# Performance work log

Measured on AMD Instinct MI355X. Metric: run time of the kernel, lower is better.

The kernel has to match this reference:

```python
import jax, jax.numpy as jnp
import numpy as np

C = 512
G = 32  # GroupNorm groups
EPS = 1e-6


def setup_inputs() -> dict:
    key = jax.random.key(0)
    ks = jax.random.split(key, 12)
    B, H, W = 2, 64, 64
    s = 0.02
    return {
        "x": jax.random.normal(ks[0], (B, C, H, W), dtype=jnp.float32),
        "gn_w": jnp.ones((C,), jnp.float32),
        "gn_b": jnp.zeros((C,), jnp.float32),
        "wq": jax.random.normal(ks[1], (C, C), jnp.float32) * s,
        "bq": jnp.zeros((C,), jnp.float32),
        "wk": jax.random.normal(ks[2], (C, C), jnp.float32) * s,
        "bk": jnp.zeros((C,), jnp.float32),
        "wv": jax.random.normal(ks[3], (C, C), jnp.float32) * s,
        "bv": jnp.zeros((C,), jnp.float32),
        "wp": jax.random.normal(ks[4], (C, C), jnp.float32) * s,
        "bp": jnp.zeros((C,), jnp.float32),
    }


def _group_norm(x, w, b):
    B, Cc, H, W = x.shape
    xg = x.reshape(B, G, Cc // G, H, W)
    mu = jnp.mean(xg, axis=(2, 3, 4), keepdims=True)
    var = jnp.var(xg, axis=(2, 3, 4), keepdims=True)
    xn = ((xg - mu) * jax.lax.rsqrt(var + EPS)).reshape(B, Cc, H, W)
    return xn * w[None, :, None, None] + b[None, :, None, None]


def reference(x, gn_w, gn_b, wq, bq, wk, bk, wv, bv, wp, bp):
    B, Cc, H, W = x.shape
    N = H * W
    h = _group_norm(x, gn_w, gn_b)
    hf = h.reshape(B, Cc, N)  # [B,C,N]
    # 1x1 conv == per-position linear over channels
    q = jnp.einsum('dc,bcn->bdn', wq, hf) + bq[None, :, None]
    k = jnp.einsum('dc,bcn->bdn', wk, hf) + bk[None, :, None]
    v = jnp.einsum('dc,bcn->bdn', wv, hf) + bv[None, :, None]
    scale = float(Cc) ** -0.5
    # scores[b,q_pos,k_pos]
    w_ = jnp.einsum('bcq,bck->bqk', q, k) * scale
    w_ = jax.nn.softmax(w_, axis=2)
    # h_[b,c,q] = sum_k v[b,c,k] * w_[b,q,k]
    o = jnp.einsum('bck,bqk->bcq', v, w_)
    o = jnp.einsum('dc,bcn->bdn', wp, o) + bp[None, :, None]
    return x + o.reshape(B, Cc, H, W)
```

## Files before the change

### kernel.cpp

```cpp
#include <hip/hip_runtime.h>


typedef unsigned short u16;
typedef unsigned int u32;
typedef unsigned char u8;
typedef float f32x4 __attribute__((ext_vector_type(4)));
typedef long l2 __attribute__((ext_vector_type(2)));

#define NPOS 4096
#define CCH 512

__device__ __forceinline__ int kperm(int k) {
  return (k & ~0x78) | ((k >> 2) & 0x18) | ((k << 2) & 0x60);
}

__device__ __forceinline__ u16 f2bf(float f) {
  u32 u = __builtin_bit_cast(u32, f);
  u += 0x7fffu + ((u >> 16) & 1u);
  return (u16)(u >> 16);
}
__device__ __forceinline__ float bf2f(u16 h) {
  u32 u = ((u32)h) << 16;
  return __builtin_bit_cast(float, u);
}
__device__ __forceinline__ u8 f2fp8(float f) {
  u32 pk = __builtin_amdgcn_cvt_pk_fp8_f32(f, f, 0, false);
  return (u8)(pk & 0xff);
}

__device__ __forceinline__ void load16_lds8(const u8* g, u8* l) {
  __builtin_amdgcn_global_load_lds(
      (const __attribute__((address_space(1))) void*)g,
      (__attribute__((address_space(3))) void*)l, 16, 0, 0);
}

__global__ __launch_bounds__(256) void gn_stats_part(const float* __restrict__ x,
                                                     float2* __restrict__ part) {
  int id = blockIdx.x;
  const float4* p = (const float4*)(x + (size_t)id * 16384);
  float s = 0.f, s2 = 0.f;
  for (int i = threadIdx.x; i < 4096; i += 256) {
    float4 u = p[i];
    s += u.x + u.y + u.z + u.w;
    s2 += u.x * u.x + u.y * u.y + u.z * u.z + u.w * u.w;
  }
  for (int o = 32; o; o >>= 1) {
    s += __shfl_xor(s, o);
    s2 += __shfl_xor(s2, o);
  }
  __shared__ float rs[4], rq[4];
  int lane = threadIdx.x & 63, w = threadIdx.x >> 6;
  if (lane == 0) { rs[w] = s; rq[w] = s2; }
  __syncthreads();
  if (threadIdx.x == 0)
    part[id] = make_float2(rs[0] + rs[1] + rs[2] + rs[3], rq[0] + rq[1] + rq[2] + rq[3]);
}

__global__ __launch_bounds__(256) void gn_apply8(const float* __restrict__ x,
                                                 const float* __restrict__ gnw,
                                                 const float* __restrict__ gnb,
                                                 const float2* __restrict__ pstats,
                                                 u8* __restrict__ h8) {
  int b = blockIdx.z, c0 = blockIdx.y * 64, n0 = blockIdx.x * 64;
  __shared__ u8 lt[64][80];
  const float* xb = x + (size_t)b * CCH * NPOS;
  int tid = threadIdx.x;
#pragma unroll
  for (int it = 0; it < 4; ++it) {
    int ci = (tid >> 4) + it * 16;
    int nj = (tid & 15) * 4;
    int c = c0 + ci;
    float4 v = *(const float4*)&xb[(size_t)c * NPOS + n0 + nj];
    const float2* pp = pstats + ((size_t)b * 32 + (c >> 4)) * 4;
    float s = pp[0].x + pp[1].x + pp[2].x + pp[3].x;
    float s2 = pp[0].y + pp[1].y + pp[2].y + pp[3].y;
    float mu = s * (1.f / 65536.f);
    float var = s2 * (1.f / 65536.f) - mu * mu;
    float rst = rsqrtf(var + 1e-6f);
    float w = gnw[c] * rst;
    float bb = gnb[c] - mu * w;
    lt[nj + 0][ci] = f2fp8(v.x * w + bb);
    lt[nj + 1][ci] = f2fp8(v.y * w + bb);
    lt[nj + 2][ci] = f2fp8(v.z * w + bb);
    lt[nj + 3][ci] = f2fp8(v.w * w + bb);
  }
  __syncthreads();
  int ni = tid >> 2, c16 = (tid & 3) * 16;
  uint4 o = *(const uint4*)&lt[ni][c16];
  u8* row = h8 + ((size_t)b * NPOS + n0 + ni) * CCH;
  int pc = kperm(c0 + c16);
  *(uint2*)&row[pc] = make_uint2(o.x, o.y);
  *(uint2*)&row[kperm(c0 + c16 + 8)] = make_uint2(o.z, o.w);
}

__global__ __launch_bounds__(256) void wconv8(const float* __restrict__ w0,
                                              const float* __restrict__ w1,
                                              const float* __restrict__ w2,
                                              const float* __restrict__ w3,
                                              u8* __restrict__ dst,
                                              const float* __restrict__ bq,
                                              const float* __restrict__ bk,
                                              const float* __restrict__ bv,
                                              float* __restrict__ bqkv) {
  int which = blockIdx.y;
  int bx = blockIdx.x;
  int t = threadIdx.x;
  if (bx == 256) {
    if (which < 3) {
      const float* bsrc = which == 0 ? bq : which == 1 ? bk : bv;
      bqkv[which * 512 + t] = bsrc[t];
      bqkv[which * 512 + 256 + t] = bsrc[256 + t];
    }
    return;
  }
  const float* src = which == 0 ? w0 : which == 1 ? w1 : which == 2 ? w2 : w3;
  u8* d = dst + (size_t)which * (CCH * CCH);
  int i = bx * 256 + t;
  float4 v = ((const float4*)src)[i];
  u32 pk = __builtin_amdgcn_cvt_pk_fp8_f32(v.x, v.y, 0, false);
  pk = __builtin_amdgcn_cvt_pk_fp8_f32(v.z, v.w, pk, true);
  int byte = i * 4;
  int c = byte & 511;
  ((u32*)d)[((byte & ~511) | kperm(c)) >> 2] = pk;
}

template <int EPI, bool SWIZ>
__global__ __launch_bounds__(256, 4) void gemm_f8(const u8* __restrict__ A,
                                                  const u8* __restrict__ Bm,
                                                  void* __restrict__ Cv,
                                                  const float* __restrict__ bias,
                                                  const float* __restrict__ resid,
                                                  float* __restrict__ lpart,
                                                  float alpha, int K,
                                                  int lda, int ldb, int ldc,
                                                  long sA, long sB, long sC, long sR) {
  const int b = blockIdx.z;
  int bx = blockIdx.x, by = blockIdx.y;
  if (SWIZ) {
    int id = by * gridDim.x + bx;
    int g = id >> 8;
    int w = id & 255;
    bx = (g << 3) | (w & 7);
    by = w >> 3;
  }
  A += (size_t)b * sA;
  Bm += (size_t)b * sB;
  const int m0 = by * 128, n0 = bx * 128;
  __shared__ u8 sAt[128 * 128];
  __shared__ u8 sBt[128 * 128];
  const int tid = threadIdx.x, wave = tid >> 6, lane = tid & 63;
  const int lrow = lane & 15, kch = lane >> 4;
  const int wm = (wave >> 1) * 64, wn = (wave & 1) * 64;
  const int srow = lane >> 3;
  const int sseg = ((lane & 7) ^ srow) * 16;
  f32x4 acc[4][4] = {};

  for (int k0 = 0; k0 < K; k0 += 128) {
#pragma unroll
    for (int r = 0; r < 4; ++r) {
      int ch = wave * 4 + r;
      load16_lds8(A + (size_t)(m0 + ch * 8 + srow) * lda + (k0 + sseg), sAt + ch * 1024);
      load16_lds8(Bm + (size_t)(n0 + ch * 8 + srow) * ldb + (k0 + sseg), sBt + ch * 1024);
    }
    __syncthreads();
#pragma unroll
    for (int kkhi = 0; kkhi < 2; ++kkhi) {
      const int slot = (kch << 1) | kkhi;
      l2 af[4], bf[4];
#pragma unroll
      for (int i = 0; i < 4; ++i) {
        int ra = wm + i * 16 + lrow;
        af[i] = *(const l2*)(sAt + ra * 128 + ((slot ^ (ra & 7)) << 4));
        int rb = wn + i * 16 + lrow;
        bf[i] = *(const l2*)(sBt + rb * 128 + ((slot ^ (rb & 7)) << 4));
      }
#pragma unroll
      for (int i = 0; i < 4; ++i)
#pragma unroll
        for (int j = 0; j < 4; ++j)
          acc[i][j] =
              __builtin_amdgcn_mfma_f32_16x16x32_fp8_fp8(af[i].x, bf[j].x, acc[i][j], 0, 0, 0);
#pragma unroll
      for (int i = 0; i < 4; ++i)
#pragma unroll
        for (int j = 0; j < 4; ++j)
          acc[i][j] =
              __builtin_amdgcn_mfma_f32_16x16x32_fp8_fp8(af[i].y, bf[j].y, acc[i][j], 0, 0, 0);
    }
    __syncthreads();
  }

  const int col = lane & 15, rbase = (lane >> 4) * 4;
  const size_t cb = (size_t)b * sC;
  float rsum[4][4];
  if (EPI == 2) {
#pragma unroll
    for (int i = 0; i < 4; ++i)
#pragma unroll
      for (int r = 0; r < 4; ++r) rsum[i][r] = 0.f;
  }
#pragma unroll
  for (int i = 0; i < 4; ++i) {
    int mrow = m0 + wm + i * 16 + rbase;
#pragma unroll
    for (int j = 0; j < 4; ++j) {
      int ncol = n0 + wn + j * 16 + col;
      float bcol = (EPI == 0) ? bias[ncol] : 0.f;
      int scol = ncol;
      if (EPI == 0 && ncol < 1024) scol = kperm(ncol);
      if (EPI == 2) scol = kperm(ncol);
#pragma unroll
      for (int r = 0; r < 4; ++r) {
        int m = mrow + r;
        float v = acc[i][j][r];
        if (EPI == 0) {
          ((u8*)Cv)[cb + (size_t)m * ldc + scol] = f2fp8(v + bcol);
        } else if (EPI == 1) {
          v = v * alpha + bias[m] + resid[(size_t)b * sR + (size_t)m * ldc + ncol];
          ((float*)Cv)[cb + (size_t)m * ldc + ncol] = v;
        } else {
          float s = fminf(fmaxf(v * alpha, -14.f), 6.49f);
          float e = exp2f(s);
          rsum[i][r] += e;
          ((u8*)Cv)[cb + (size_t)m * ldc + scol] = f2fp8(4.f * e);
        }
      }
    }
  }
  if (EPI == 2) {
#pragma unroll
    for (int i = 0; i < 4; ++i) {
#pragma unroll
      for (int r = 0; r < 4; ++r) {
        float v = rsum[i][r];
        v += __shfl_xor(v, 1);
        v += __shfl_xor(v, 2);
        v += __shfl_xor(v, 4);
        v += __shfl_xor(v, 8);
        if ((lane & 15) == 0) {
          int m = m0 + wm + i * 16 + rbase + r;
          lpart[((size_t)b * NPOS + m) * 64 + bx * 2 + (wave & 1)] = v;
        }
      }
    }
  }
}

__global__ __launch_bounds__(256, 4) void gemm_pv_fp8(const u8* __restrict__ Um,
                                                      const u8* __restrict__ Vm,
                                                      u16* __restrict__ part,
                                                      const float* __restrict__ lpart,
                                                      float* __restrict__ lsum) {
  const int b = blockIdx.z >> 2, slice = blockIdx.z & 3;
  const int id = blockIdx.x + (blockIdx.y << 2);
  const int xcd = id & 7, j = id >> 3;
  const int bx = j & 3, by = xcd + ((j >> 2) << 3);
  const u8* A = Um + (size_t)b * ((size_t)NPOS * NPOS) + (size_t)slice * 1024;
  const u8* Bv = Vm + (size_t)b * (CCH * NPOS) + (size_t)slice * 1024;
  const int m0 = by * 128, n0 = bx * 128;
  __shared__ u8 sA[128 * 128];
  __shared__ u8 sB[128 * 128];
  const int tid = threadIdx.x, wave = tid >> 6, lane = tid & 63;
  const int lrow = lane & 15, kch = lane >> 4;
  const int wm = (wave >> 1) * 64, wn = (wave & 1) * 64;
  const int srow = lane >> 3;
  const int sseg = ((lane & 7) ^ srow) * 16;
  f32x4 acc[4][4] = {};

  for (int k0 = 0; k0 < 1024; k0 += 128) {
#pragma unroll
    for (int r = 0; r < 4; ++r) {
      int ch = wave * 4 + r;
      load16_lds8(A + (size_t)(m0 + ch * 8 + srow) * NPOS + (k0 + sseg), sA + ch * 1024);
      load16_lds8(Bv + (size_t)(n0 + ch * 8 + srow) * NPOS + (k0 + sseg), sB + ch * 1024);
    }
    __syncthreads();
#pragma unroll
    for (int kkhi = 0; kkhi < 2; ++kkhi) {
      const int slot = (kch << 1) | kkhi;
      l2 af[4], bf[4];
#pragma unroll
      for (int i = 0; i < 4; ++i) {
        int ra = wm + i * 16 + lrow;
        af[i] = *(const l2*)(sA + ra * 128 + ((slot ^ (ra & 7)) << 4));
        int rb = wn + i * 16 + lrow;
        bf[i] = *(const l2*)(sB + rb * 128 + ((slot ^ (rb & 7)) << 4));
      }
#pragma unroll
      for (int i = 0; i < 4; ++i)
#pragma unroll
        for (int jj = 0; jj < 4; ++jj)
          acc[i][jj] =
              __builtin_amdgcn_mfma_f32_16x16x32_fp8_fp8(af[i].x, bf[jj].x, acc[i][jj], 0, 0, 0);
#pragma unroll
      for (int i = 0; i < 4; ++i)
#pragma unroll
        for (int jj = 0; jj < 4; ++jj)
          acc[i][jj] =
              __builtin_amdgcn_mfma_f32_16x16x32_fp8_fp8(af[i].y, bf[jj].y, acc[i][jj], 0, 0, 0);
    }
    __syncthreads();
  }

  const int col = lane & 15, rbase = (lane >> 4) * 4;
  u16* dst = part + (size_t)slice * ((size_t)2 * NPOS * CCH) + (size_t)b * (NPOS * CCH);
#pragma unroll
  for (int i = 0; i < 4; ++i) {
    int mrow = m0 + wm + i * 16 + rbase;
#pragma unroll
    for (int jj = 0; jj < 4; ++jj) {
      int ncol = n0 + wn + jj * 16 + col;
#pragma unroll
      for (int r = 0; r < 4; ++r)
        dst[(size_t)(mrow + r) * CCH + ncol] = f2bf(acc[i][jj][r]);
    }
  }
  if (bx == 0 && tid < 128) {
    const float* lp = lpart + ((size_t)b * NPOS + m0 + tid) * 64;
    float s = 0.f;
#pragma unroll
    for (int c = 0; c < 64; ++c) s += lp[c];
    lsum[(size_t)b * NPOS + m0 + tid] = s;
  }
}

__global__ __launch_bounds__(256) void merge_pv8(const u16* __restrict__ part,
                                                 const float* __restrict__ lsum,
                                                 u8* __restrict__ dst) {
  const long sl = 4194304;
  int i = blockIdx.x * 256 + threadIdx.x;
  long e0 = (long)i * 8;
  int q = (int)((e0 >> 9) & 4095);
  int b = (int)(e0 >> 21);
  int c8 = (int)(e0 & 511);
  float inv = 8.f / lsum[(size_t)b * NPOS + q];
  uint4 a = ((const uint4*)part)[i];
  uint4 bb = ((const uint4*)(part + sl))[i];
  uint4 c = ((const uint4*)(part + 2 * sl))[i];
  uint4 d = ((const uint4*)(part + 3 * sl))[i];
  u32 wa[4] = {a.x, a.y, a.z, a.w}, wb_[4] = {bb.x, bb.y, bb.z, bb.w};
  u32 wc[4] = {c.x, c.y, c.z, c.w}, wd[4] = {d.x, d.y, d.z, d.w};
  float v[8];
#pragma unroll
  for (int j = 0; j < 4; ++j) {
    v[2 * j] = (bf2f((u16)(wa[j] & 0xffff)) + bf2f((u16)(wb_[j] & 0xffff)) +
                bf2f((u16)(wc[j] & 0xffff)) + bf2f((u16)(wd[j] & 0xffff))) * inv;
    v[2 * j + 1] = (bf2f((u16)(wa[j] >> 16)) + bf2f((u16)(wb_[j] >> 16)) +
                    bf2f((u16)(wc[j] >> 16)) + bf2f((u16)(wd[j] >> 16))) * inv;
  }
  uint2 o;
  u32 p0 = __builtin_amdgcn_cvt_pk_fp8_f32(v[0], v[1], 0, false);
  p0 = __builtin_amdgcn_cvt_pk_fp8_f32(v[2], v[3], p0, true);
  u32 p1 = __builtin_amdgcn_cvt_pk_fp8_f32(v[4], v[5], 0, false);
  p1 = __builtin_amdgcn_cvt_pk_fp8_f32(v[6], v[7], p1, true);
  o.x = p0;
  o.y = p1;
  *(uint2*)&dst[((size_t)b * NPOS + q) * CCH + kperm(c8)] = o;
}

__global__ __launch_bounds__(256) void transpose_v8(const u8* __restrict__ src,
                                                    u8* __restrict__ dst, int srcld) {
  int b = blockIdx.z, n0 = blockIdx.x * 64, d0 = blockIdx.y * 64;
  __shared__ u8 lt[64][80];
  const u8* s = src + (size_t)b * NPOS * srcld;
  u8* d = dst + (size_t)b * CCH * NPOS;
  int t = threadIdx.x;
  {
    int r = t >> 2, c16 = (t & 3) * 16;
    uint4 v = *(const uint4*)&s[(size_t)(n0 + r) * srcld + d0 + c16];
    *(uint4*)&lt[r][c16] = v;
  }
  __syncthreads();
  {
    int dr = t >> 2, c16 = (t & 3) * 16;
    u8 tmp[16];
#pragma unroll
    for (int j = 0; j < 16; ++j) tmp[j] = lt[c16 + j][dr];
    uint4 o = *(uint4*)tmp;
    u8* row = d + (size_t)(d0 + dr) * NPOS;
    *(uint2*)&row[kperm(n0 + c16)] = make_uint2(o.x, o.y);
    *(uint2*)&row[kperm(n0 + c16 + 8)] = make_uint2(o.z, o.w);
  }
}

extern "C" void kernel_launch(void* const* d_in, const int* in_sizes, int n_in,
                              void* d_out, int out_size, void* d_ws, size_t ws_size,
                              hipStream_t stream) {
  const float* x = (const float*)d_in[0];
  const float* gnw = (const float*)d_in[1];
  const float* gnb = (const float*)d_in[2];
  const float* wq = (const float*)d_in[3];
  const float* bq = (const float*)d_in[4];
  const float* wk = (const float*)d_in[5];
  const float* bk = (const float*)d_in[6];
  const float* wv = (const float*)d_in[7];
  const float* bv = (const float*)d_in[8];
  const float* wp = (const float*)d_in[9];
  const float* bp = (const float*)d_in[10];
  float* out = (float*)d_out;

  char* ws = (char*)d_ws;
  size_t off = 0;
  auto alloc = [&](size_t bytes) {
    void* p = ws + off;
    off += (bytes + 1023) & ~(size_t)1023;
    return p;
  };
  float2* pstats = (float2*)alloc(256 * sizeof(float2));
  u8* w8 = (u8*)alloc((size_t)4 * CCH * CCH);
  u8* wp8 = w8 + 3 * CCH * CCH;
  float* bqkv = (float*)alloc(1536 * sizeof(float));
  u8* h8 = (u8*)alloc((size_t)2 * NPOS * CCH);
  u8* qkv8 = (u8*)alloc((size_t)2 * NPOS * 1536);
  u8* v8 = (u8*)alloc((size_t)2 * CCH * NPOS);
  u8* U8 = (u8*)alloc((size_t)2 * NPOS * NPOS);
  float* lpart = (float*)alloc((size_t)2 * NPOS * 64 * 4);
  float* lsum = (float*)alloc((size_t)2 * NPOS * 4);
  u16* part_pv = (u16*)alloc((size_t)4 * 2 * NPOS * CCH * 2);
  u8* o8 = (u8*)alloc((size_t)2 * NPOS * CCH);

  const long sHC8 = (long)NPOS * CCH;
  const long sQKV8 = (long)NPOS * 1536;
  const long sSS8 = (long)NPOS * NPOS;
  const long sOUT = (long)CCH * NPOS;
  const float scale2 = 0.044194173824159216f * 1.4426950408889634f;

  gn_stats_part<<<256, 256, 0, stream>>>(x, pstats);
  gn_apply8<<<dim3(64, 8, 2), 256, 0, stream>>>(x, gnw, gnb, pstats, h8);
  wconv8<<<dim3(257, 4), 256, 0, stream>>>(wq, wk, wv, wp, w8, bq, bk, bv, bqkv);
  gemm_f8<0, false><<<dim3(12, 32, 2), 256, 0, stream>>>(
      h8, w8, qkv8, bqkv, nullptr, nullptr, 1.f, CCH, CCH, CCH, 1536,
      sHC8, 0, sQKV8, 0);
  transpose_v8<<<dim3(64, 8, 2), 256, 0, stream>>>(qkv8 + 1024, v8, 1536);
  gemm_f8<2, true><<<dim3(32, 32, 2), 256, 0, stream>>>(
      qkv8, qkv8 + 512, U8, nullptr, nullptr, lpart, scale2, CCH, 1536, 1536, NPOS,
      sQKV8, sQKV8, sSS8, 0);
  gemm_pv_fp8<<<dim3(4, 32, 8), 256, 0, stream>>>(U8, v8, part_pv, lpart, lsum);
  merge_pv8<<<2048, 256, 0, stream>>>(part_pv, lsum, o8);
  gemm_f8<1, false><<<dim3(32, 4, 2), 256, 0, stream>>>(
      wp8, o8, out, bp, x, nullptr, 1.f / 32.f, CCH, CCH, CCH, NPOS,
      0, sHC8, sOUT, sOUT);
}
```

Measured before the change: 200.9 us.

## Use 32x32x64 scaled MFMA with pre-tiled fragment layouts for attention GEMMs

Replaces the 16x16x32 fp8 MFMA kernels for QK^T and PV with a new gemm_mx kernel that uses the MI355 scaled 32x32x64 f8f6f4 MFMA instruction. Q, K, V-transposed and the score matrix are written directly in a fragment-tiled layout (f32i), so LDS staging is a straight contiguous copy and each lane reads its 32-byte fragment without swizzling. This is meant to raise MFMA throughput and simplify address math, in exchange for extra layout-specific scattered writes in producer epilogues. The lower exp clamp in the softmax epilogue is also dropped.

```diff
diff --git a/kernel.cpp b/kernel.cpp
--- a/kernel.cpp
+++ b/kernel.cpp
@@ -5,6 +5,8 @@
 typedef unsigned int u32;
 typedef unsigned char u8;
 typedef float f32x4 __attribute__((ext_vector_type(4)));
+typedef float f32x16 __attribute__((ext_vector_type(16)));
+typedef int i32x8 __attribute__((ext_vector_type(8)));
 typedef long l2 __attribute__((ext_vector_type(2)));
 
 #define NPOS 4096
@@ -12,6 +14,10 @@
 
 __device__ __forceinline__ int kperm(int k) {
   return (k & ~0x78) | ((k >> 2) & 0x18) | ((k << 2) & 0x60);
+}
+__device__ __forceinline__ int f32i(int R, int C, int KBT) {
+  return ((R >> 5) * KBT + (C >> 6)) * 2048 + ((R & 31) + ((C >> 5) & 1) * 32) * 32 +
+         (C & 31);
 }
 
 __device__ __forceinline__ u16 f2bf(float f) {
@@ -88,8 +94,7 @@
   int ni = tid >> 2, c16 = (tid & 3) * 16;
   uint4 o = *(const uint4*)&lt[ni][c16];
   u8* row = h8 + ((size_t)b * NPOS + n0 + ni) * CCH;
-  int pc = kperm(c0 + c16);
-  *(uint2*)&row[pc] = make_uint2(o.x, o.y);
+  *(uint2*)&row[kperm(c0 + c16)] = make_uint2(o.x, o.y);
   *(uint2*)&row[kperm(c0 + c16 + 8)] = make_uint2(o.z, o.w);
 }
 
@@ -124,25 +129,19 @@
   ((u32*)d)[((byte & ~511) | kperm(c)) >> 2] = pk;
 }
 
-template <int EPI, bool SWIZ>
+template <int EPI>
 __global__ __launch_bounds__(256, 4) void gemm_f8(const u8* __restrict__ A,
                                                   const u8* __restrict__ Bm,
                                                   void* __restrict__ Cv,
+                                                  u8* __restrict__ pq,
+                                                  u8* __restrict__ pk,
                                                   const float* __restrict__ bias,
                                                   const float* __restrict__ resid,
-                                                  float* __restrict__ lpart,
                                                   float alpha, int K,
                                                   int lda, int ldb, int ldc,
                                                   long sA, long sB, long sC, long sR) {
   const int b = blockIdx.z;
   int bx = blockIdx.x, by = blockIdx.y;
-  if (SWIZ) {
-    int id = by * gridDim.x + bx;
-    int g = id >> 8;
-    int w = id & 255;
-    bx = (g << 3) | (w & 7);
-    by = w >> 3;
-  }
   A += (size_t)b * sA;
   Bm += (size_t)b * sB;
   const int m0 = by * 128, n0 = bx * 128;
@@ -191,14 +190,6 @@
   }
 
   const int col = lane & 15, rbase = (lane >> 4) * 4;
-  const size_t cb = (size_t)b * sC;
-  float rsum[4][4];
-  if (EPI == 2) {
-#pragma unroll
-    for (int i = 0; i < 4; ++i)
-#pragma unroll
-      for (int r = 0; r < 4; ++r) rsum[i][r] = 0.f;
-  }
 #pragma unroll
   for (int i = 0; i < 4; ++i) {
     int mrow = m0 + wm + i * 16 + rbase;
@@ -206,116 +197,134 @@
     for (int j = 0; j < 4; ++j) {
       int ncol = n0 + wn + j * 16 + col;
       float bcol = (EPI == 0) ? bias[ncol] : 0.f;
-      int scol = ncol;
-      if (EPI == 0 && ncol < 1024) scol = kperm(ncol);
-      if (EPI == 2) scol = kperm(ncol);
 #pragma unroll
       for (int r = 0; r < 4; ++r) {
         int m = mrow + r;
         float v = acc[i][j][r];
         if (EPI == 0) {
-          ((u8*)Cv)[cb + (size_t)m * ldc + scol] = f2fp8(v + bcol);
-        } else if (EPI == 1) {
+          u8 e = f2fp8(v + bcol);
+          if (ncol < 512)
+            pq[(size_t)b * (NPOS * CCH) + f32i(m, ncol, 8)] = e;
+          else if (ncol < 1024)
+            pk[(size_t)b * (NPOS * CCH) + f32i(m, ncol - 512, 8)] = e;
+          else
+            ((u8*)Cv)[(size_t)b * (NPOS * CCH) + (size_t)m * 512 + (ncol - 1024)] = e;
+        } else {
           v = v * alpha + bias[m] + resid[(size_t)b * sR + (size_t)m * ldc + ncol];
-          ((float*)Cv)[cb + (size_t)m * ldc + ncol] = v;
-        } else {
-          float s = fminf(fmaxf(v * alpha, -14.f), 6.49f);
-          float e = exp2f(s);
-          rsum[i][r] += e;
-          ((u8*)Cv)[cb + (size_t)m * ldc + scol] = f2fp8(4.f * e);
+          ((float*)Cv)[(size_t)b * sC + (size_t)m * ldc + ncol] = v;
         }
       }
     }
   }
-  if (EPI == 2) {
-#pragma unroll
-    for (int i = 0; i < 4; ++i) {
-#pragma unroll
-      for (int r = 0; r < 4; ++r) {
-        float v = rsum[i][r];
-        v += __shfl_xor(v, 1);
-        v += __shfl_xor(v, 2);
-        v += __shfl_xor(v, 4);
-        v += __shfl_xor(v, 8);
-        if ((lane & 15) == 0) {
-          int m = m0 + wm + i * 16 + rbase + r;
-          lpart[((size_t)b * NPOS + m) * 64 + bx * 2 + (wave & 1)] = v;
+}
+
+template <int EPI, bool SWIZ, bool XCD>
+__global__ __launch_bounds__(256, 4) void gemm_mx(const u8* __restrict__ A,
+                                                  const u8* __restrict__ Bm,
+                                                  void* __restrict__ Cv,
+                                                  float* __restrict__ lpart,
+                                                  float* __restrict__ lsum,
+                                                  float alpha, int ktiles,
+                                                  int kbtA, int kbtB, int kbOffUnit,
+                                                  long sA, long sB) {
+  int b, slice, bx, by;
+  if (XCD) {
+    b = blockIdx.z >> 2;
+    slice = blockIdx.z & 3;
+    const int id = blockIdx.x + (blockIdx.y << 2);
+    const int xcd = id & 7, j = id >> 3;
+    bx = j & 3;
+    by = xcd + ((j >> 2) << 3);
+  } else {
+    b = blockIdx.z;
+    slice = 0;
+    bx = blockIdx.x;
+    by = blockIdx.y;
+    if (SWIZ) {
+      int id = by * gridDim.x + bx;
+      int g = id >> 8;
+      int w = id & 255;
+      bx = (g << 3) | (w & 7);
+      by = w >> 3;
+    }
+  }
+  const int kbOff = slice * kbOffUnit;
+  const u8* Ab = A + (size_t)b * sA;
+  const u8* Bb = Bm + (size_t)b * sB;
+  const int m0 = by * 128, n0 = bx * 128;
+  __shared__ u8 sAt[16384];
+  __shared__ u8 sBt[16384];
+  const int tid = threadIdx.x, wave = tid >> 6, lane = tid & 63;
+  f32x16 acc[2][2] = {};
+
+  for (int kt = 0; kt < ktiles; ++kt) {
+#pragma unroll
+    for (int kbl = 0; kbl < 2; ++kbl)
+#pragma unroll
+      for (int half = 0; half < 2; ++half) {
+        const u8* ga = Ab + (size_t)((by * 4 + wave) * kbtA + kbOff + kt * 2 + kbl) * 2048 +
+                       half * 1024 + lane * 16;
+        load16_lds8(ga, sAt + (wave * 2 + kbl) * 2048 + half * 1024 + lane * 16);
+        const u8* gb = Bb + (size_t)((bx * 4 + wave) * kbtB + kbOff + kt * 2 + kbl) * 2048 +
+                       half * 1024 + lane * 16;
+        load16_lds8(gb, sBt + (wave * 2 + kbl) * 2048 + half * 1024 + lane * 16);
+      }
+    __syncthreads();
+#pragma unroll
+    for (int kbl = 0; kbl < 2; ++kbl) {
+      i32x8 af[2], bf[2];
+#pragma unroll
+      for (int i = 0; i < 2; ++i)
+        af[i] = *(const i32x8*)(sAt + ((((wave >> 1) * 2 + i) * 2 + kbl) * 2048) + lane * 32);
+#pragma unroll
+      for (int j = 0; j < 2; ++j)
+        bf[j] = *(const i32x8*)(sBt + ((((wave & 1) * 2 + j) * 2 + kbl) * 2048) + lane * 32);
+#pragma unroll
+      for (int i = 0; i < 2; ++i)
+#pragma unroll
+        for (int j = 0; j < 2; ++j)
+          acc[i][j] = __builtin_amdgcn_mfma_scale_f32_32x32x64_f8f6f4(
+              af[i], bf[j], acc[i][j], 0, 0, 0, 127, 0, 127);
+    }
+    __syncthreads();
+  }
+
+  const int h = lane >> 5, c31 = lane & 31;
+#pragma unroll
+  for (int i = 0; i < 2; ++i) {
+    const int mbase = m0 + (wave >> 1) * 64 + i * 32;
+#pragma unroll
+    for (int r = 0; r < 16; ++r) {
+      const int ro = (r & 3) + ((r >> 2) << 3) + (h << 2);
+      const int m = mbase + ro;
+      if (EPI == 2) {
+        float rowsum = 0.f;
+#pragma unroll
+        for (int j = 0; j < 2; ++j) {
+          int ncol = n0 + (wave & 1) * 64 + j * 32 + c31;
+          float e = exp2f(fminf(acc[i][j][r] * alpha, 6.49f));
+          rowsum += e;
+          ((u8*)Cv)[(size_t)b * ((size_t)NPOS * NPOS) + f32i(m, ncol, 64)] = f2fp8(4.f * e);
+        }
+        rowsum += __shfl_xor(rowsum, 1);
+        rowsum += __shfl_xor(rowsum, 2);
+        rowsum += __shfl_xor(rowsum, 4);
+        rowsum += __shfl_xor(rowsum, 8);
+        rowsum += __shfl_xor(rowsum, 16);
+        if (c31 == 0)
+          lpart[((size_t)b * NPOS + m) * 64 + bx * 2 + (wave & 1)] = rowsum;
+      } else {
+        u16* dst = (u16*)Cv + (size_t)slice * ((size_t)2 * NPOS * CCH) +
+                   (size_t)b * (NPOS * CCH);
+#pragma unroll
+        for (int j = 0; j < 2; ++j) {
+          int ncol = n0 + (wave & 1) * 64 + j * 32 + c31;
+          dst[(size_t)m * CCH + ncol] = f2bf(acc[i][j][r]);
         }
       }
     }
   }
-}
-
-__global__ __launch_bounds__(256, 4) void gemm_pv_fp8(const u8* __restrict__ Um,
-                                                      const u8* __restrict__ Vm,
-                                                      u16* __restrict__ part,
-                                                      const float* __restrict__ lpart,
-                                                      float* __restrict__ lsum) {
-  const int b = blockIdx.z >> 2, slice = blockIdx.z & 3;
-  const int id = blockIdx.x + (blockIdx.y << 2);
-  const int xcd = id & 7, j = id >> 3;
-  const int bx = j & 3, by = xcd + ((j >> 2) << 3);
-  const u8* A = Um + (size_t)b * ((size_t)NPOS * NPOS) + (size_t)slice * 1024;
-  const u8* Bv = Vm + (size_t)b * (CCH * NPOS) + (size_t)slice * 1024;
-  const int m0 = by * 128, n0 = bx * 128;
-  __shared__ u8 sA[128 * 128];
-  __shared__ u8 sB[128 * 128];
-  const int tid = threadIdx.x, wave = tid >> 6, lane = tid & 63;
-  const int lrow = lane & 15, kch = lane >> 4;
-  const int wm = (wave >> 1) * 64, wn = (wave & 1) * 64;
-  const int srow = lane >> 3;
-  const int sseg = ((lane & 7) ^ srow) * 16;
-  f32x4 acc[4][4] = {};
-
-  for (int k0 = 0; k0 < 1024; k0 += 128) {
-#pragma unroll
-    for (int r = 0; r < 4; ++r) {
-      int ch = wave * 4 + r;
-      load16_lds8(A + (size_t)(m0 + ch * 8 + srow) * NPOS + (k0 + sseg), sA + ch * 1024);
-      load16_lds8(Bv + (size_t)(n0 + ch * 8 + srow) * NPOS + (k0 + sseg), sB + ch * 1024);
-    }
-    __syncthreads();
-#pragma unroll
-    for (int kkhi = 0; kkhi < 2; ++kkhi) {
-      const int slot = (kch << 1) | kkhi;
-      l2 af[4], bf[4];
-#pragma unroll
-      for (int i = 0; i < 4; ++i) {
-        int ra = wm + i * 16 + lrow;
-        af[i] = *(const l2*)(sA + ra * 128 + ((slot ^ (ra & 7)) << 4));
-        int rb = wn + i * 16 + lrow;
-        bf[i] = *(const l2*)(sB + rb * 128 + ((slot ^ (rb & 7)) << 4));
-      }
-#pragma unroll
-      for (int i = 0; i < 4; ++i)
-#pragma unroll
-        for (int jj = 0; jj < 4; ++jj)
-          acc[i][jj] =
-              __builtin_amdgcn_mfma_f32_16x16x32_fp8_fp8(af[i].x, bf[jj].x, acc[i][jj], 0, 0, 0);
-#pragma unroll
-      for (int i = 0; i < 4; ++i)
-#pragma unroll
-        for (int jj = 0; jj < 4; ++jj)
-          acc[i][jj] =
-              __builtin_amdgcn_mfma_f32_16x16x32_fp8_fp8(af[i].y, bf[jj].y, acc[i][jj], 0, 0, 0);
-    }
-    __syncthreads();
-  }
-
-  const int col = lane & 15, rbase = (lane >> 4) * 4;
-  u16* dst = part + (size_t)slice * ((size_t)2 * NPOS * CCH) + (size_t)b * (NPOS * CCH);
-#pragma unroll
-  for (int i = 0; i < 4; ++i) {
-    int mrow = m0 + wm + i * 16 + rbase;
-#pragma unroll
-    for (int jj = 0; jj < 4; ++jj) {
-      int ncol = n0 + wn + jj * 16 + col;
-#pragma unroll
-      for (int r = 0; r < 4; ++r)
-        dst[(size_t)(mrow + r) * CCH + ncol] = f2bf(acc[i][jj][r]);
-    }
-  }
-  if (bx == 0 && tid < 128) {
+  if (EPI == 3 && bx == 0 && tid < 128) {
     const float* lp = lpart + ((size_t)b * NPOS + m0 + tid) * 64;
     float s = 0.f;
 #pragma unroll
@@ -359,15 +368,15 @@
 }
 
 __global__ __launch_bounds__(256) void transpose_v8(const u8* __restrict__ src,
-                                                    u8* __restrict__ dst, int srcld) {
+                                                    u8* __restrict__ dst) {
   int b = blockIdx.z, n0 = blockIdx.x * 64, d0 = blockIdx.y * 64;
   __shared__ u8 lt[64][80];
-  const u8* s = src + (size_t)b * NPOS * srcld;
-  u8* d = dst + (size_t)b * CCH * NPOS;
+  const u8* s = src + (size_t)b * NPOS * CCH;
+  u8* d = dst + (size_t)b * (CCH * NPOS);
   int t = threadIdx.x;
   {
     int r = t >> 2, c16 = (t & 3) * 16;
-    uint4 v = *(const uint4*)&s[(size_t)(n0 + r) * srcld + d0 + c16];
+    uint4 v = *(const uint4*)&s[(size_t)(n0 + r) * CCH + d0 + c16];
     *(uint4*)&lt[r][c16] = v;
   }
   __syncthreads();
@@ -376,10 +385,7 @@
     u8 tmp[16];
 #pragma unroll
     for (int j = 0; j < 16; ++j) tmp[j] = lt[c16 + j][dr];
-    uint4 o = *(uint4*)tmp;
-    u8* row = d + (size_t)(d0 + dr) * NPOS;
-    *(uint2*)&row[kperm(n0 + c16)] = make_uint2(o.x, o.y);
-    *(uint2*)&row[kperm(n0 + c16 + 8)] = make_uint2(o.z, o.w);
+    *(uint4*)&d[f32i(d0 + dr, n0 + c16, 64)] = *(uint4*)tmp;
   }
 }
 
@@ -411,7 +417,9 @@
   u8* wp8 = w8 + 3 * CCH * CCH;
   float* bqkv = (float*)alloc(1536 * sizeof(float));
   u8* h8 = (u8*)alloc((size_t)2 * NPOS * CCH);
-  u8* qkv8 = (u8*)alloc((size_t)2 * NPOS * 1536);
+  u8* q8 = (u8*)alloc((size_t)2 * NPOS * CCH);
+  u8* k8 = (u8*)alloc((size_t)2 * NPOS * CCH);
+  u8* vtmp = (u8*)alloc((size_t)2 * NPOS * CCH);
   u8* v8 = (u8*)alloc((size_t)2 * CCH * NPOS);
   u8* U8 = (u8*)alloc((size_t)2 * NPOS * NPOS);
   float* lpart = (float*)alloc((size_t)2 * NPOS * 64 * 4);
@@ -420,7 +428,6 @@
   u8* o8 = (u8*)alloc((size_t)2 * NPOS * CCH);
 
   const long sHC8 = (long)NPOS * CCH;
-  const long sQKV8 = (long)NPOS * 1536;
   const long sSS8 = (long)NPOS * NPOS;
   const long sOUT = (long)CCH * NPOS;
   const float scale2 = 0.044194173824159216f * 1.4426950408889634f;
@@ -428,16 +435,16 @@
   gn_stats_part<<<256, 256, 0, stream>>>(x, pstats);
   gn_apply8<<<dim3(64, 8, 2), 256, 0, stream>>>(x, gnw, gnb, pstats, h8);
   wconv8<<<dim3(257, 4), 256, 0, stream>>>(wq, wk, wv, wp, w8, bq, bk, bv, bqkv);
-  gemm_f8<0, false><<<dim3(12, 32, 2), 256, 0, stream>>>(
-      h8, w8, qkv8, bqkv, nullptr, nullptr, 1.f, CCH, CCH, CCH, 1536,
-      sHC8, 0, sQKV8, 0);
-  transpose_v8<<<dim3(64, 8, 2), 256, 0, stream>>>(qkv8 + 1024, v8, 1536);
-  gemm_f8<2, true><<<dim3(32, 32, 2), 256, 0, stream>>>(
-      qkv8, qkv8 + 512, U8, nullptr, nullptr, lpart, scale2, CCH, 1536, 1536, NPOS,
-      sQKV8, sQKV8, sSS8, 0);
-  gemm_pv_fp8<<<dim3(4, 32, 8), 256, 0, stream>>>(U8, v8, part_pv, lpart, lsum);
+  gemm_f8<0><<<dim3(12, 32, 2), 256, 0, stream>>>(
+      h8, w8, vtmp, q8, k8, bqkv, nullptr, 1.f, CCH, CCH, CCH, 1536,
+      sHC8, 0, 0, 0);
+  transpose_v8<<<dim3(64, 8, 2), 256, 0, stream>>>(vtmp, v8);
+  gemm_mx<2, true, false><<<dim3(32, 32, 2), 256, 0, stream>>>(
+      q8, k8, U8, lpart, nullptr, scale2, 4, 8, 8, 0, sHC8, sHC8);
+  gemm_mx<3, false, true><<<dim3(4, 32, 8), 256, 0, stream>>>(
+      U8, v8, part_pv, lpart, lsum, 1.f, 8, 64, 64, 16, sSS8, sHC8);
   merge_pv8<<<2048, 256, 0, stream>>>(part_pv, lsum, o8);
-  gemm_f8<1, false><<<dim3(32, 4, 2), 256, 0, stream>>>(
-      wp8, o8, out, bp, x, nullptr, 1.f / 32.f, CCH, CCH, CCH, NPOS,
+  gemm_f8<1><<<dim3(32, 4, 2), 256, 0, stream>>>(
+      wp8, o8, out, nullptr, nullptr, bp, x, 1.f / 32.f, CCH, CCH, CCH, NPOS,
       0, sHC8, sOUT, sOUT);
 }
```

Result: slower. 207.3 us (+3.2%).
